# Kernel tuning notes

Hardware: AMD Instinct MI355X
Metric: run time of the kernel (lower is better)

## Reference

```python
import jax, jax.numpy as jnp
import numpy as np

N_NODES = 100000
N_EDGES = 3200000
IN_F, HID_F, OUT_F = 512, 64, 16


def setup_inputs() -> dict:
    key = jax.random.key(0)
    k1, k2, k3, k4 = jax.random.split(key, 4)
    x = jax.random.normal(k1, (N_NODES, IN_F), dtype=jnp.float32)
    edge_index = jax.random.randint(k2, (2, N_EDGES), 0, N_NODES, dtype=jnp.int64)
    W1 = jax.random.normal(k3, (IN_F, HID_F), dtype=jnp.float32) * (1.0 / np.sqrt(IN_F))
    b1 = jnp.zeros((HID_F,), dtype=jnp.float32)
    W2 = jax.random.normal(k4, (HID_F, OUT_F), dtype=jnp.float32) * (1.0 / np.sqrt(HID_F))
    b2 = jnp.zeros((OUT_F,), dtype=jnp.float32)
    return {"x": x, "edge_index": edge_index, "W1": W1, "b1": b1, "W2": W2, "b2": b2}


def _gcn_norm(edge_index, n_nodes):
    # add self-loops (GCNConv default), edge_weight = 1
    loop = jnp.arange(n_nodes, dtype=edge_index.dtype)
    src = jnp.concatenate([edge_index[0], loop])
    dst = jnp.concatenate([edge_index[1], loop])
    ones = jnp.ones(src.shape[0], dtype=jnp.float32)
    deg = jax.ops.segment_sum(ones, dst, num_segments=n_nodes)
    dinv = jnp.where(deg > 0, jax.lax.rsqrt(deg), 0.0)
    norm = dinv[src] * dinv[dst]  # symmetric normalization D^-1/2 A D^-1/2
    return src, dst, norm


def _gcn_conv(h, src, dst, norm, W, b, n_nodes):
    h = h @ W                                 # project first (small GEMM)
    msg = h[src] * norm[:, None]              # gather + scale  [E+N, F_out]
    agg = jax.ops.segment_sum(msg, dst, num_segments=n_nodes)  # scatter-add
    return agg + b


def reference(x, edge_index, W1, b1, W2, b2):
    n = x.shape[0]
    src, dst, norm = _gcn_norm(edge_index, n)
    h = jax.nn.relu(_gcn_conv(x, src, dst, norm, W1, b1, n))
    # F.dropout with training=False is identity (eval-mode reference)
    h = _gcn_conv(h, src, dst, norm, W2, b2, n)
    return jax.nn.log_softmax(h, axis=1)
```

## Files before the change

kernel.cpp:

```cpp
#include <hip/hip_runtime.h>

#define NN    100000
#define NE    3200000
#define INF_  512
#define HIDF  64
#define OUTF  16
#define BR    128
#define NBUCK ((NN + BR - 1) / BR)
#define NGRP  8
#define SLICE 704
#define BSLOT (NGRP * SLICE)
#define NCUR  (NBUCK * NGRP)
#define NSLOT 72
#define EBLK  16384
#define NFB   ((NE + EBLK - 1) / EBLK)
#define GM    64
#define NGB   ((NN + GM - 1) / GM)

typedef __bf16 bf16x8 __attribute__((ext_vector_type(8)));
typedef float  f32x4  __attribute__((ext_vector_type(4)));

__device__ inline unsigned short f2bfu(float f) {
    unsigned u = __builtin_bit_cast(unsigned, f);
    u += 0x7FFFu + ((u >> 16) & 1u);
    return (unsigned short)(u >> 16);
}
__device__ inline __bf16 bfbits(unsigned short h) {
    return __builtin_bit_cast(__bf16, h);
}
__device__ inline float bf2f(unsigned short h) {
    unsigned u = (unsigned)h << 16;
    return __builtin_bit_cast(float, u);
}

__global__ __launch_bounds__(256) void k_prep(const float* __restrict__ W1,
                                              unsigned short* __restrict__ w1c,
                                              int* __restrict__ bcur) {
    int b = blockIdx.x, t = threadIdx.x;
    if (b < 128) {
        int i = b * 256 + t;
        int k = i >> 6, n = i & 63;
        w1c[((k >> 2) * 64 + n) * 4 + (k & 3)] = f2bfu(W1[i]);
    } else {
        int i = (b - 128) * 256 + t;
        if (i < NCUR) bcur[i] = (i >> 3) * BSLOT + (i & 7) * SLICE;
    }
}

__global__ __launch_bounds__(256) void k_main(const float* __restrict__ x,
                                              const unsigned short* __restrict__ w1c,
                                              const int* __restrict__ src,
                                              const int* __restrict__ dst,
                                              int* __restrict__ bcur,
                                              unsigned int* __restrict__ pairs,
                                              unsigned short* __restrict__ h1s) {
    __shared__ __align__(16) char smem[16384];
    int t = threadIdx.x;

    if (blockIdx.x < NFB) {
        int* hist  = (int*)smem;
        int* rbase = ((int*)smem) + NBUCK;
        int e0 = blockIdx.x * EBLK;
        int e1 = (e0 + EBLK < NE) ? e0 + EBLK : NE;
        int grp = (int)(((long long)blockIdx.x * NGRP) / NFB);

        for (int b = t; b < NBUCK; b += 256) hist[b] = 0;
        __syncthreads();
        for (int e = e0 + t; e < e1; e += 256)
            atomicAdd(&hist[dst[e] >> 7], 1);
        __syncthreads();
        for (int b = t; b < NBUCK; b += 256) {
            int c = hist[b];
            rbase[b] = c ? atomicAdd(&bcur[b * NGRP + grp], c) : 0;
            hist[b] = 0;
        }
        __syncthreads();
        for (int e = e0 + t; e < e1; e += 256) {
            int s = src[e], d = dst[e];
            int b = d >> 7;
            int slot = atomicAdd(&hist[b], 1);
            pairs[rbase[b] + slot] = ((unsigned)s << 7) | (unsigned)(d & 127);
        }
        return;
    }

    unsigned short* bs = (unsigned short*)smem;
    int lane = t & 63;
    int w    = t >> 6;
    int m    = lane & 15;
    int kg   = lane >> 4;
    int mb   = (blockIdx.x - NFB) * GM;

    int rowi = mb + w * 16 + m;
    size_t xrow = (size_t)((rowi < NN) ? rowi : NN - 1);
    const float* xp = x + xrow * INF_ + kg * 4;

    f32x4 acc0 = {0.f,0.f,0.f,0.f}, acc1 = acc0, acc2 = acc0, acc3 = acc0;

    const uint4* w1c4 = (const uint4*)w1c;
    uint4* bs4 = (uint4*)bs;

    for (int kc = 0; kc < 4; ++kc) {
#pragma unroll
        for (int i = 0; i < 4; ++i)
            bs4[t + i * 256] = w1c4[kc * 1024 + t + i * 256];
        __syncthreads();

#pragma unroll
        for (int ks = 0; ks < 4; ++ks) {
            int ksg = kc * 4 + ks;
            float4 xa = *(const float4*)(xp + ksg * 32);
            float4 xb = *(const float4*)(xp + ksg * 32 + 16);
            bf16x8 A;
            A[0] = bfbits(f2bfu(xa.x)); A[1] = bfbits(f2bfu(xa.y));
            A[2] = bfbits(f2bfu(xa.z)); A[3] = bfbits(f2bfu(xa.w));
            A[4] = bfbits(f2bfu(xb.x)); A[5] = bfbits(f2bfu(xb.y));
            A[6] = bfbits(f2bfu(xb.z)); A[7] = bfbits(f2bfu(xb.w));

            int qq0 = ks * 8 + kg;
            int qq1 = qq0 + 4;
#pragma unroll
            for (int n0t = 0; n0t < 4; ++n0t) {
                ushort4 b0 = *(const ushort4*)&bs[(qq0 * 64 + n0t * 16 + m) * 4];
                ushort4 b1 = *(const ushort4*)&bs[(qq1 * 64 + n0t * 16 + m) * 4];
                bf16x8 B;
                B[0] = bfbits(b0.x); B[1] = bfbits(b0.y);
                B[2] = bfbits(b0.z); B[3] = bfbits(b0.w);
                B[4] = bfbits(b1.x); B[5] = bfbits(b1.y);
                B[6] = bfbits(b1.z); B[7] = bfbits(b1.w);
                f32x4 c = (n0t == 0) ? acc0 : (n0t == 1) ? acc1 : (n0t == 2) ? acc2 : acc3;
                c = __builtin_amdgcn_mfma_f32_16x16x32_bf16(A, B, c, 0, 0, 0);
                if      (n0t == 0) acc0 = c;
                else if (n0t == 1) acc1 = c;
                else if (n0t == 2) acc2 = c;
                else               acc3 = c;
            }
        }
        __syncthreads();
    }

#pragma unroll
    for (int r = 0; r < 4; ++r) {
        int node = mb + w * 16 + kg * 4 + r;
        if (node < NN) {
            size_t o = (size_t)node * HIDF + m;
            h1s[o +  0] = f2bfu(acc0[r]);
            h1s[o + 16] = f2bfu(acc1[r]);
            h1s[o + 32] = f2bfu(acc2[r]);
            h1s[o + 48] = f2bfu(acc3[r]);
        }
    }
}

__global__ __launch_bounds__(256) void k_fillB(const int* __restrict__ bcur,
                                               const unsigned int* __restrict__ pairs,
                                               int* __restrict__ re,
                                               float* __restrict__ dinv,
                                               int* __restrict__ csr,
                                               unsigned short* __restrict__ h1s) {
    __shared__ int   cur_s[BR];
    __shared__ float dinv_s[BR];
    int b  = blockIdx.x;
    int t  = threadIdx.x;
    int n0 = b * BR;
    int ncount = ((n0 + BR < NN) ? BR : NN - n0);

    if (t < BR) cur_s[t] = (n0 + t) * NSLOT;
    __syncthreads();

    for (int g = 0; g < NGRP; ++g) {
        int s0 = b * BSLOT + g * SLICE;
        int s1 = bcur[b * NGRP + g];
        for (int j = s0 + t; j < s1; j += 256) {
            unsigned int p = pairs[j];
            int pos = atomicAdd(&cur_s[p & 127u], 1);
            csr[pos] = (int)(p >> 7);
        }
    }
    __syncthreads();

    if (t < ncount) {
        int endp = cur_s[t];
        int n = n0 + t;
        float dv = rsqrtf((float)(endp - n * NSLOT + 1));
        re[n]    = endp;
        dinv[n]  = dv;
        dinv_s[t] = dv;
    }
    __syncthreads();

    for (int i = t; i < ncount * HIDF; i += 256) {
        unsigned idx = (unsigned)(n0 * HIDF + i);
        h1s[idx] = f2bfu(bf2f(h1s[idx]) * dinv_s[i >> 6]);
    }
}

__global__ __launch_bounds__(256) void k_hid2(const int* __restrict__ re,
                                              const int* __restrict__ csr,
                                              const float* __restrict__ dinv,
                                              const unsigned short* __restrict__ h1s,
                                              const float* __restrict__ b1,
                                              const float* __restrict__ W2,
                                              unsigned short* __restrict__ h2s) {
    __shared__ float w2s[HIDF * OUTF];
    __shared__ float b1s[HIDF];
    __shared__ float hbuf[4][HIDF];
    int t = threadIdx.x;
    for (int i = t; i < HIDF * OUTF; i += 256) w2s[i] = W2[i];
    if (t < HIDF) b1s[t] = b1[t];
    __syncthreads();

    int l = t & 63;
    int w = t >> 6;
    int g = l >> 4;
    int q = l & 15;
    int n = __builtin_amdgcn_readfirstlane(blockIdx.x * 4 + w);
    int row = n * NSLOT;
    int end = re[n];
    float dn = dinv[n];

    float a0 = 0.f, a1 = 0.f, a2 = 0.f, a3 = 0.f;

    int j = row;
    for (; j + 16 <= end; j += 16) {
        int4 scA = *(const int4*)&csr[j];
        int4 scB = *(const int4*)&csr[j + 4];
        int4 scC = *(const int4*)&csr[j + 8];
        int4 scD = *(const int4*)&csr[j + 12];
        int sA = (g & 2) ? ((g & 1) ? scA.w : scA.z) : ((g & 1) ? scA.y : scA.x);
        int sB = (g & 2) ? ((g & 1) ? scB.w : scB.z) : ((g & 1) ? scB.y : scB.x);
        int sC = (g & 2) ? ((g & 1) ? scC.w : scC.z) : ((g & 1) ? scC.y : scC.x);
        int sD = (g & 2) ? ((g & 1) ? scD.w : scD.z) : ((g & 1) ? scD.y : scD.x);
        ushort4 hA = *(const ushort4*)&h1s[(unsigned)(sA * HIDF + q * 4)];
        ushort4 hB = *(const ushort4*)&h1s[(unsigned)(sB * HIDF + q * 4)];
        ushort4 hC = *(const ushort4*)&h1s[(unsigned)(sC * HIDF + q * 4)];
        ushort4 hD = *(const ushort4*)&h1s[(unsigned)(sD * HIDF + q * 4)];
        a0 += (bf2f(hA.x) + bf2f(hB.x)) + (bf2f(hC.x) + bf2f(hD.x));
        a1 += (bf2f(hA.y) + bf2f(hB.y)) + (bf2f(hC.y) + bf2f(hD.y));
        a2 += (bf2f(hA.z) + bf2f(hB.z)) + (bf2f(hC.z) + bf2f(hD.z));
        a3 += (bf2f(hA.w) + bf2f(hB.w)) + (bf2f(hC.w) + bf2f(hD.w));
    }
    for (; j + 8 <= end; j += 8) {
        int4 scA = *(const int4*)&csr[j];
        int4 scB = *(const int4*)&csr[j + 4];
        int sA = (g & 2) ? ((g & 1) ? scA.w : scA.z) : ((g & 1) ? scA.y : scA.x);
        int sB = (g & 2) ? ((g & 1) ? scB.w : scB.z) : ((g & 1) ? scB.y : scB.x);
        ushort4 hA = *(const ushort4*)&h1s[(unsigned)(sA * HIDF + q * 4)];
        ushort4 hB = *(const ushort4*)&h1s[(unsigned)(sB * HIDF + q * 4)];
        a0 += bf2f(hA.x) + bf2f(hB.x);
        a1 += bf2f(hA.y) + bf2f(hB.y);
        a2 += bf2f(hA.z) + bf2f(hB.z);
        a3 += bf2f(hA.w) + bf2f(hB.w);
    }
    if (j + 4 <= end) {
        int4 sc = *(const int4*)&csr[j];
        int s = (g & 2) ? ((g & 1) ? sc.w : sc.z) : ((g & 1) ? sc.y : sc.x);
        ushort4 h = *(const ushort4*)&h1s[(unsigned)(s * HIDF + q * 4)];
        a0 += bf2f(h.x); a1 += bf2f(h.y); a2 += bf2f(h.z); a3 += bf2f(h.w);
        j += 4;
    }
    if (j + g < end) {
        int s = csr[j + g];
        ushort4 h = *(const ushort4*)&h1s[(unsigned)(s * HIDF + q * 4)];
        a0 += bf2f(h.x); a1 += bf2f(h.y); a2 += bf2f(h.z); a3 += bf2f(h.w);
    }

    a0 += __shfl_xor(a0, 16); a1 += __shfl_xor(a1, 16);
    a2 += __shfl_xor(a2, 16); a3 += __shfl_xor(a3, 16);
    a0 += __shfl_xor(a0, 32); a1 += __shfl_xor(a1, 32);
    a2 += __shfl_xor(a2, 32); a3 += __shfl_xor(a3, 32);

    ushort4 hs = *(const ushort4*)&h1s[(unsigned)(n * HIDF + q * 4)];
    a0 = fmaxf(fmaf(dn, a0 + bf2f(hs.x), b1s[q * 4 + 0]), 0.f);
    a1 = fmaxf(fmaf(dn, a1 + bf2f(hs.y), b1s[q * 4 + 1]), 0.f);
    a2 = fmaxf(fmaf(dn, a2 + bf2f(hs.z), b1s[q * 4 + 2]), 0.f);
    a3 = fmaxf(fmaf(dn, a3 + bf2f(hs.w), b1s[q * 4 + 3]), 0.f);
    if (g == 0) *(float4*)&hbuf[w][q * 4] = make_float4(a0, a1, a2, a3);
    __syncthreads();

    int o  = l & 15;
    int kg = l >> 4;
    const float* hb = hbuf[w];
    float s = 0.f;
#pragma unroll
    for (int i = 0; i < 16; ++i) {
        int k = kg * 16 + i;
        s = fmaf(hb[k], w2s[k * OUTF + o], s);
    }
    s += __shfl_xor(s, 16);
    s += __shfl_xor(s, 32);
    if (l < 16) h2s[(unsigned)(n * OUTF + o)] = f2bfu(dn * s);
}

__global__ __launch_bounds__(256) void k_out2(const int* __restrict__ re,
                                              const int* __restrict__ csr,
                                              const float* __restrict__ dinv,
                                              const unsigned short* __restrict__ h2s,
                                              const float* __restrict__ b2,
                                              float* __restrict__ out) {
    int t = blockIdx.x * 256 + threadIdx.x;
    int n = t >> 4;
    int f = t & 15;
    if (n >= NN) return;
    int row = n * NSLOT, end = re[n];
    float dn = dinv[n];
    float acc = bf2f(h2s[(unsigned)(n * OUTF + f)]);

    int j = row;
    for (; j + 8 <= end; j += 8) {
        int s0 = csr[j],     s1 = csr[j + 1], s2 = csr[j + 2], s3 = csr[j + 3];
        int s4 = csr[j + 4], s5 = csr[j + 5], s6 = csr[j + 6], s7 = csr[j + 7];
        float v0 = bf2f(h2s[(unsigned)(s0 * OUTF + f)]);
        float v1 = bf2f(h2s[(unsigned)(s1 * OUTF + f)]);
        float v2 = bf2f(h2s[(unsigned)(s2 * OUTF + f)]);
        float v3 = bf2f(h2s[(unsigned)(s3 * OUTF + f)]);
        float v4 = bf2f(h2s[(unsigned)(s4 * OUTF + f)]);
        float v5 = bf2f(h2s[(unsigned)(s5 * OUTF + f)]);
        float v6 = bf2f(h2s[(unsigned)(s6 * OUTF + f)]);
        float v7 = bf2f(h2s[(unsigned)(s7 * OUTF + f)]);
        acc += ((v0 + v1) + (v2 + v3)) + ((v4 + v5) + (v6 + v7));
    }
    for (; j + 4 <= end; j += 4) {
        int s0 = csr[j], s1 = csr[j + 1], s2 = csr[j + 2], s3 = csr[j + 3];
        float v0 = bf2f(h2s[(unsigned)(s0 * OUTF + f)]);
        float v1 = bf2f(h2s[(unsigned)(s1 * OUTF + f)]);
        float v2 = bf2f(h2s[(unsigned)(s2 * OUTF + f)]);
        float v3 = bf2f(h2s[(unsigned)(s3 * OUTF + f)]);
        acc += (v0 + v1) + (v2 + v3);
    }
    for (; j < end; ++j)
        acc += bf2f(h2s[(unsigned)(csr[j] * OUTF + f)]);

    float v = fmaf(dn, acc, b2[f]);

    float m = v;
#pragma unroll
    for (int mask = 1; mask < 16; mask <<= 1)
        m = fmaxf(m, __shfl_xor(m, mask, 16));
    float ex = __expf(v - m);
    float s  = ex;
#pragma unroll
    for (int mask = 1; mask < 16; mask <<= 1)
        s += __shfl_xor(s, mask, 16);
    out[(size_t)n * OUTF + f] = v - (m + __logf(s));
}

extern "C" void kernel_launch(void* const* d_in, const int* in_sizes, int n_in,
                              void* d_out, int out_size, void* d_ws, size_t ws_size,
                              hipStream_t stream) {
    const float* x  = (const float*)d_in[0];
    const int*   ei = (const int*)d_in[1];
    const float* W1 = (const float*)d_in[2];
    const float* b1 = (const float*)d_in[3];
    const float* W2 = (const float*)d_in[4];
    const float* b2 = (const float*)d_in[5];
    float*       out = (float*)d_out;

    char*  ws = (char*)d_ws;
    size_t o  = 0;
    auto alloc = [&](size_t bytes) {
        void* p = ws + o;
        o = (o + bytes + 1023) & ~(size_t)1023;
        return p;
    };
    int*            bcur  = (int*)           alloc((size_t)NCUR * 4);
    int*            re    = (int*)           alloc((size_t)NN * 4);
    int*            csr   = (int*)           alloc((size_t)NN * NSLOT * 4);
    unsigned int*   pairs = (unsigned int*)  alloc((size_t)NBUCK * BSLOT * 4);
    float*          dinv  = (float*)         alloc((size_t)NN * 4);
    unsigned short* w1c   = (unsigned short*)alloc((size_t)INF_ * HIDF * 2);
    unsigned short* h1s   = (unsigned short*)alloc((size_t)NN * HIDF * 2);
    unsigned short* h2s   = (unsigned short*)alloc((size_t)NN * OUTF * 2);
    if (o > ws_size) return;

    const int* esrc = ei;
    const int* edst = ei + NE;

    k_prep  <<<128 + (NCUR + 255) / 256, 256, 0, stream>>>(W1, w1c, bcur);
    k_main  <<<NFB + NGB, 256, 0, stream>>>(x, w1c, esrc, edst, bcur, pairs, h1s);
    k_fillB <<<NBUCK, 256, 0, stream>>>(bcur, pairs, re, dinv, csr, h1s);
    k_hid2  <<<NN / 4, 256, 0, stream>>>(re, csr, dinv, h1s, b1, W2, h2s);
    k_out2  <<<(NN * OUTF + 255) / 256, 256, 0, stream>>>(re, csr, dinv, h2s, b2, out);
}
```

Baseline: 247.2 us.

## Stage x tiles into LDS via global_load_lds with XOR swizzle

Instead of each lane loading its x fragments directly from global memory with strided float4 reads, each K-chunk of the 64-row x tile is now copied into a swizzled LDS buffer using the asynchronous global_load_lds path. MFMA A operands are then read from LDS, with an XOR swizzle to avoid bank conflicts. The aim is coalesced, wide global reads for the dominant 200MB x read. In exchange, LDS use grows to 48KB per block, which may reduce occupancy, and there is no double buffering, so load latency is still exposed at each barrier.

```diff
diff --git a/kernel.cpp b/kernel.cpp
--- a/kernel.cpp
+++ b/kernel.cpp
@@ -33,6 +33,13 @@
     return __builtin_bit_cast(float, u);
 }
 
+__device__ inline void gll16(const float* g, void* l) {
+    __builtin_amdgcn_global_load_lds(
+        (const __attribute__((address_space(1))) unsigned int*)g,
+        (__attribute__((address_space(3))) unsigned int*)l,
+        16, 0, 0);
+}
+
 __global__ __launch_bounds__(256) void k_prep(const float* __restrict__ W1,
                                               unsigned short* __restrict__ w1c,
                                               int* __restrict__ bcur) {
@@ -54,7 +61,7 @@
                                               int* __restrict__ bcur,
                                               unsigned int* __restrict__ pairs,
                                               unsigned short* __restrict__ h1s) {
-    __shared__ __align__(16) char smem[16384];
+    __shared__ __align__(16) char smem[49152];
     int t = threadIdx.x;
 
     if (blockIdx.x < NFB) {
@@ -85,15 +92,18 @@
     }
 
     unsigned short* bs = (unsigned short*)smem;
+    float*          xt = (float*)(smem + 16384);
     int lane = t & 63;
-    int w    = t >> 6;
+    int w    = __builtin_amdgcn_readfirstlane(t >> 6);
     int m    = lane & 15;
     int kg   = lane >> 4;
     int mb   = (blockIdx.x - NFB) * GM;
 
-    int rowi = mb + w * 16 + m;
-    size_t xrow = (size_t)((rowi < NN) ? rowi : NN - 1);
-    const float* xp = x + xrow * INF_ + kg * 4;
+    int rl_half = lane >> 5;
+    int segl    = lane & 31;
+
+    int rA = w * 16 + m;
+    int swz = rA & 7;
 
     f32x4 acc0 = {0.f,0.f,0.f,0.f}, acc1 = acc0, acc2 = acc0, acc3 = acc0;
 
@@ -101,21 +111,30 @@
     uint4* bs4 = (uint4*)bs;
 
     for (int kc = 0; kc < 4; ++kc) {
+        if (kc) __syncthreads();
 #pragma unroll
         for (int i = 0; i < 4; ++i)
             bs4[t + i * 256] = w1c4[kc * 1024 + t + i * 256];
+#pragma unroll
+        for (int i = 0; i < 8; ++i) {
+            int rloc = w * 16 + i * 2 + rl_half;
+            int rg   = mb + rloc; if (rg >= NN) rg = NN - 1;
+            int sseg = segl ^ (rloc & 7);
+            const float* gp = x + (size_t)rg * INF_ + kc * 128 + sseg * 4;
+            gll16(gp, (char*)xt + (w * 8192 + i * 1024));
+        }
         __syncthreads();
 
 #pragma unroll
         for (int ks = 0; ks < 4; ++ks) {
-            int ksg = kc * 4 + ks;
-            float4 xa = *(const float4*)(xp + ksg * 32);
-            float4 xb = *(const float4*)(xp + ksg * 32 + 16);
+            int s0g = ks * 8 + kg;
+            float4 xa  = *(const float4*)&xt[rA * 128 + ((s0g ^ swz) << 2)];
+            float4 xbv = *(const float4*)&xt[rA * 128 + (((s0g + 4) ^ swz) << 2)];
             bf16x8 A;
-            A[0] = bfbits(f2bfu(xa.x)); A[1] = bfbits(f2bfu(xa.y));
-            A[2] = bfbits(f2bfu(xa.z)); A[3] = bfbits(f2bfu(xa.w));
-            A[4] = bfbits(f2bfu(xb.x)); A[5] = bfbits(f2bfu(xb.y));
-            A[6] = bfbits(f2bfu(xb.z)); A[7] = bfbits(f2bfu(xb.w));
+            A[0] = bfbits(f2bfu(xa.x));  A[1] = bfbits(f2bfu(xa.y));
+            A[2] = bfbits(f2bfu(xa.z));  A[3] = bfbits(f2bfu(xa.w));
+            A[4] = bfbits(f2bfu(xbv.x)); A[5] = bfbits(f2bfu(xbv.y));
+            A[6] = bfbits(f2bfu(xbv.z)); A[7] = bfbits(f2bfu(xbv.w));
 
             int qq0 = ks * 8 + kg;
             int qq1 = qq0 + 4;
@@ -136,7 +155,6 @@
                 else               acc3 = c;
             }
         }
-        __syncthreads();
     }
 
 #pragma unroll
```

Result: no change. 246.7 us (-0.2%).
